# Kernel tuning notes

Hardware: AMD Instinct MI355X
Metric: run time of the kernel (lower is better)

The kernel has to match this reference:

```python
import jax, jax.numpy as jnp
import numpy as np

B = 64        # number of graph segments
BASE = 384    # mean verts per segment
LMAX = 512    # pad length (counts in [256, 512])
H_DIM = 256
H_DIV = 128   # h_dim // h_dim_div
HEADS = 4
DH = H_DIV // HEADS  # 32


def _counts(seed):
    rng = np.random.default_rng(seed)
    d = rng.integers(-128, 129, B)
    d[1::2] = -d[::2]            # paired so the total is exactly B*BASE
    return (BASE + d).astype(np.int64)


def _pad_indices(counts, L):
    # Gather indices/mask mapping packed ragged tokens -> padded [B, L].
    counts = np.asarray(counts)
    off = np.concatenate([[0], np.cumsum(counts)[:-1]])
    ar = np.arange(L)[None, :]
    mask = ar < counts[:, None]
    idx = np.where(mask, off[:, None] + ar, 0)
    return idx, mask


def setup_inputs() -> dict:
    key = jax.random.key(0)
    ks = jax.random.split(key, 16)
    src_num_verts = _counts(0)
    dst_num_verts = _counts(1)
    total = B * BASE  # 24576 for both src and dst

    def w(k, shape):
        return 0.02 * jax.random.normal(k, shape, jnp.float32)

    return {
        'src_h': jax.random.normal(ks[0], (total, H_DIM), jnp.float32),
        'dst_h': jax.random.normal(ks[1], (total, H_DIM), jnp.float32),
        'src_num_verts': src_num_verts,
        'dst_num_verts': dst_num_verts,
        # 1x1 Conv1d == linear over channels
        'Wq': w(ks[2], (H_DIV, H_DIM)), 'bq': w(ks[3], (H_DIV,)),
        'Wk': w(ks[4], (H_DIV, H_DIM)), 'bk': w(ks[5], (H_DIV,)),
        'Wv': w(ks[6], (H_DIV, H_DIM)), 'bv': w(ks[7], (H_DIV,)),
        'Wm': w(ks[8], (H_DIV, H_DIV)), 'bm': w(ks[9], (H_DIV,)),
        'W1': w(ks[10], (H_DIM, H_DIM + H_DIV)), 'b1': w(ks[11], (H_DIM,)),
        'g1': 1.0 + 0.1 * jax.random.normal(ks[12], (H_DIM,), jnp.float32),
        'be1': w(ks[13], (H_DIM,)),
        'rm1': w(ks[14], (H_DIM,)),
        'rv1': jax.random.uniform(ks[15], (H_DIM,), jnp.float32, 0.5, 1.5),
        'W2': w(jax.random.fold_in(key, 100), (H_DIM, H_DIM)),
        'b2': w(jax.random.fold_in(key, 101), (H_DIM,)),
        'g2': 1.0 + 0.1 * jax.random.normal(jax.random.fold_in(key, 102), (H_DIM,), jnp.float32),
        'be2': w(jax.random.fold_in(key, 103), (H_DIM,)),
        'rm2': w(jax.random.fold_in(key, 104), (H_DIM,)),
        'rv2': jax.random.uniform(jax.random.fold_in(key, 105), (H_DIM,), jnp.float32, 0.5, 1.5),
    }


def _bn(x, g, b, rm, rv):
    # BatchNorm1d in eval mode (running stats)
    return (x - rm) / jnp.sqrt(rv + 1e-5) * g + b


def reference(src_h, dst_h, src_num_verts, dst_num_verts,
              Wq, bq, Wk, bk, Wv, bv, Wm, bm,
              W1, b1, g1, be1, rm1, rv1,
              W2, b2, g2, be2, rm2, rv2):
    didx, dmask = _pad_indices(dst_num_verts, LMAX)
    sidx, smask = _pad_indices(src_num_verts, LMAX)

    # fused projections over all packed tokens (1x1 conv == matmul)
    q = src_h_proj = dst_h @ Wq.T + bq        # [Nd, H_DIV]
    k = src_h @ Wk.T + bk                     # [Ns, H_DIV]
    v = src_h @ Wv.T + bv

    # pad to block-diagonal batched form; channel c = d*HEADS + h per torch view
    qp = q[didx].reshape(B, LMAX, DH, HEADS)
    kp = k[sidx].reshape(B, LMAX, DH, HEADS)
    vp = v[sidx].reshape(B, LMAX, DH, HEADS)

    scores = jnp.einsum('bndh,bmdh->bhnm', qp, kp) / (DH ** 0.5)
    scores = jnp.where(jnp.asarray(smask)[:, None, None, :], scores, -1e9)
    attn = jax.nn.softmax(scores, axis=-1)
    msg = jnp.einsum('bhnm,bmdh->bndh', attn, vp).reshape(B, LMAX, H_DIV)
    msg = msg @ Wm.T + bm                     # merge conv

    bb, ii = np.nonzero(dmask)                # unpad back to packed layout
    h_msg = msg[bb, ii]                       # [Nd, H_DIV]

    x = jnp.concatenate([dst_h, h_msg], axis=-1)
    x = _bn(x @ W1.T + b1, g1, be1, rm1, rv1)
    x = jax.nn.relu(x)
    x = _bn(x @ W2.T + b2, g2, be2, rm2, rv2)
    return dst_h + x
```

## Files before the change

kernel.cpp:

```cpp
#include <hip/hip_runtime.h>
#include <hip/hip_bf16.h>
#include <math.h>

#define B_SEG 64
#define HDIM 256
#define HDIV 128
#define NHEADS 4
#define DH 32
#define KSTR 40
#define VSTR 520
#define PSTR 136
#define QSC 0.17677669529663687f

typedef unsigned short u16;
typedef unsigned int u32;

typedef __attribute__((ext_vector_type(8))) short s8v;
typedef __attribute__((ext_vector_type(4))) float f4v;

__device__ __forceinline__ u16 f2bf(float f) {
    u32 v;
    __builtin_memcpy(&v, &f, 4);
    u32 r = v + 0x7fffu + ((v >> 16) & 1u);
    return (u16)(r >> 16);
}

__device__ __forceinline__ void async_cp16(const u16* g, u16* l) {
    __builtin_amdgcn_global_load_lds(
        (const __attribute__((address_space(1))) u32*)g,
        (__attribute__((address_space(3))) u32*)l, 16, 0, 0);
}

__global__ __launch_bounds__(256) void k_prep(
    const float* __restrict__ Wq, const float* __restrict__ bq,
    const float* __restrict__ Wk, const float* __restrict__ bk,
    const float* __restrict__ Wv, const float* __restrict__ bv,
    const float* __restrict__ Wm, const float* __restrict__ bm,
    const float* __restrict__ W1, const float* __restrict__ b1,
    const float* __restrict__ g1, const float* __restrict__ be1,
    const float* __restrict__ rm1, const float* __restrict__ rv1,
    const float* __restrict__ W2, const float* __restrict__ b2,
    const float* __restrict__ g2, const float* __restrict__ be2,
    const float* __restrict__ rm2, const float* __restrict__ rv2,
    const int* __restrict__ sc_raw, const int* __restrict__ dc_raw,
    const float* __restrict__ src_h, const float* __restrict__ dst_h,
    int* __restrict__ meta,
    u16* __restrict__ pWq, u16* __restrict__ pWkv,
    u16* __restrict__ pW1f, u16* __restrict__ pW2,
    float* __restrict__ bqp, float* __restrict__ bkvp,
    float* __restrict__ sc1, float* __restrict__ sh1,
    float* __restrict__ sc2, float* __restrict__ sh2,
    u16* __restrict__ srcb, u16* __restrict__ dstb, int ntot) {
    if (blockIdx.x < 1028) {
        int idx = blockIdx.x * 256 + threadIdx.x;
        if (idx < 32768) {
            int cp = idx >> 8, k = idx & 255;
            int c = ((cp & 31) << 2) | (cp >> 5);
            pWq[idx] = f2bf(Wq[c * 256 + k]);
        } else if (idx < 98304) {
            int i = idx - 32768;
            int rp = i >> 8, k = i & 255;
            int r = rp & 127;
            int c = ((r & 31) << 2) | (r >> 5);
            float v = (rp < 128) ? Wk[c * 256 + k] : Wv[c * 256 + k];
            pWkv[i] = f2bf(v);
        } else if (idx < 163840) {
            int i = idx - 98304;
            int o = i >> 8, k = i & 255;
            pW1f[o * 384 + k] = f2bf(W1[o * 384 + k]);
        } else if (idx < 196608) {
            int i = idx - 163840;
            int o = i >> 7, cp = i & 127;
            int c = ((cp & 31) << 2) | (cp >> 5);
            float acc = 0.f;
            for (int j = 0; j < 128; j++)
                acc += W1[o * 384 + 256 + j] * Wm[j * 128 + c];
            pW1f[o * 384 + 256 + cp] = f2bf(acc);
        } else if (idx < 262144) {
            int i = idx - 196608;
            pW2[i] = f2bf(W2[i]);
        } else if (idx < 263168) {
            int p = idx - 262144;
            if (p < 128) {
                int c = ((p & 31) << 2) | (p >> 5);
                bqp[p] = bq[c] * QSC;
            } else if (p < 384) {
                int r = p - 128; int rr = r & 127;
                int c = ((rr & 31) << 2) | (rr >> 5);
                bkvp[r] = (r < 128) ? bk[c] : bv[c];
            } else if (p < 640) {
                int o = p - 384;
                float bsum = 0.f;
                for (int j = 0; j < 128; j++)
                    bsum += W1[o * 384 + 256 + j] * bm[j];
                float s = g1[o] * rsqrtf(rv1[o] + 1e-5f);
                sc1[o] = s;
                sh1[o] = (b1[o] + bsum - rm1[o]) * s + be1[o];
            } else if (p < 896) {
                int o = p - 640;
                float s = g2[o] * rsqrtf(rv2[o] + 1e-5f);
                sc2[o] = s;
                sh2[o] = (b2[o] - rm2[o]) * s + be2[o];
            }
        }
    } else if (blockIdx.x == 1028) {
        if (threadIdx.x == 0) {
            bool is64 = (sc_raw[1] == 0);
            int so = 0, dofs = 0;
            for (int i = 0; i < B_SEG; i++) {
                int s = is64 ? sc_raw[2 * i] : sc_raw[i];
                int d = is64 ? dc_raw[2 * i] : dc_raw[i];
                meta[i] = s; meta[64 + i] = d;
                meta[128 + i] = so; meta[192 + i] = dofs;
                so += s; dofs += d;
            }
        }
    } else {
        int i = (blockIdx.x - 1029) * 256 + threadIdx.x;
        int half = ntot * 64;
        const float4* s;
        u16* o;
        int j = i;
        if (i < half) { s = (const float4*)src_h; o = srcb; }
        else { s = (const float4*)dst_h; o = dstb; j = i - half; }
        float4 v = s[j];
        ushort4 u = {f2bf(v.x), f2bf(v.y), f2bf(v.z), f2bf(v.w)};
        ((ushort4*)o)[j] = u;
    }
}

__device__ __forceinline__ void gemm_body(
    const u16* __restrict__ A, int lda,
    const u16* __restrict__ A2, int lda2, int K1,
    const u16* __restrict__ Bw, int K, int m0, int n0,
    const float* __restrict__ scale, const float* __restrict__ shift,
    const float* __restrict__ resid,
    void* __restrict__ Cout, int ldc, int flags,
    u16* Al, u16* Bl) {
    int tid = threadIdx.x;
    int w = tid >> 6, lane = tid & 63;
    int wm = w & 1, wn = w >> 1;
    int l15 = lane & 15, quad = lane >> 4;
    int srow = w * 32 + (lane >> 2);
    int scol = (lane & 3) << 3;
    u16* al0 = Al + w * 1024;
    u16* bl0 = Bl + w * 1024;
    f4v acc[4][4] = {};

    for (int k0 = 0; k0 < K; k0 += 32) {
        const u16* Ag; int aL, acol;
        if (k0 < K1) { Ag = A; aL = lda; acol = k0; }
        else { Ag = A2; aL = lda2; acol = k0 - K1; }
        async_cp16(&Ag[(size_t)(m0 + srow) * aL + acol + scol], al0);
        async_cp16(&Ag[(size_t)(m0 + srow + 16) * aL + acol + scol], al0 + 512);
        async_cp16(&Bw[(size_t)(n0 + srow) * K + k0 + scol], bl0);
        async_cp16(&Bw[(size_t)(n0 + srow + 16) * K + k0 + scol], bl0 + 512);
        __syncthreads();
        s8v af[4], bf[4];
#pragma unroll
        for (int i = 0; i < 4; i++)
            af[i] = *(const s8v*)(&Al[(wm * 64 + i * 16 + l15) * 32 + quad * 8]);
#pragma unroll
        for (int j = 0; j < 4; j++)
            bf[j] = *(const s8v*)(&Bl[(wn * 64 + j * 16 + l15) * 32 + quad * 8]);
#pragma unroll
        for (int i = 0; i < 4; i++)
#pragma unroll
            for (int j = 0; j < 4; j++)
                acc[i][j] = __builtin_amdgcn_mfma_f32_16x16x32_bf16(
                    af[i], bf[j], acc[i][j], 0, 0, 0);
        __syncthreads();
    }
#pragma unroll
    for (int i = 0; i < 4; i++) {
#pragma unroll
        for (int j = 0; j < 4; j++) {
            int n = n0 + wn * 64 + j * 16 + l15;
            float sc = scale ? scale[n] : 1.f;
            float sh = shift ? shift[n] : 0.f;
#pragma unroll
            for (int r = 0; r < 4; r++) {
                int m = m0 + wm * 64 + i * 16 + quad * 4 + r;
                float v = acc[i][j][r];
                if (flags & 4) v *= QSC;
                v = v * sc + sh;
                if (flags & 1) v = fmaxf(v, 0.f);
                if (resid) v += resid[(size_t)m * 256 + n];
                if (flags & 2) ((float*)Cout)[(size_t)m * ldc + n] = v;
                else ((u16*)Cout)[(size_t)m * ldc + n] = f2bf(v);
            }
        }
    }
}

__global__ __launch_bounds__(256) void k_qkv(
    const u16* __restrict__ dstb, const u16* __restrict__ srcb,
    const u16* __restrict__ pWq, const u16* __restrict__ pWkv,
    const float* __restrict__ bqp, const float* __restrict__ bkvp,
    u16* __restrict__ qb, u16* __restrict__ kvb) {
    __shared__ u16 Al[4096];
    __shared__ u16 Bl[4096];
    int m0 = blockIdx.x * 128;
    if (blockIdx.y == 0)
        gemm_body(dstb, 256, dstb, 256, 256, pWq, 256, m0, 0,
                  nullptr, bqp, nullptr, qb, 128, 4, Al, Bl);
    else
        gemm_body(srcb, 256, srcb, 256, 256, pWkv, 256, m0, (blockIdx.y - 1) * 128,
                  nullptr, bkvp, nullptr, kvb, 256, 0, Al, Bl);
}

__global__ __launch_bounds__(256) void k_gemm(
    const u16* __restrict__ A, int lda,
    const u16* __restrict__ A2, int lda2, int K1,
    const u16* __restrict__ Bw, int K,
    const float* __restrict__ scale, const float* __restrict__ shift,
    const float* __restrict__ resid,
    void* __restrict__ Cout, int ldc, int flags) {
    __shared__ u16 Al[4096];
    __shared__ u16 Bl[4096];
    gemm_body(A, lda, A2, lda2, K1, Bw, K, blockIdx.x * 128, blockIdx.y * 128,
              scale, shift, resid, Cout, ldc, flags, Al, Bl);
}

__global__ __launch_bounds__(512, 2) void k_attn(
    const u16* __restrict__ qb, const u16* __restrict__ kvb,
    const int* __restrict__ meta, u16* __restrict__ msgb) {
    extern __shared__ u16 sm[];
    u16* Kl = sm;
    u16* Vl = sm + 512 * KSTR;
    u16* Pl = Vl + 32 * VSTR;
    int b = blockIdx.x, h = blockIdx.y;
    int ns = meta[b], nd = meta[64 + b];
    int soff = meta[128 + b], doff = meta[192 + b];
    int tid = threadIdx.x, w = tid >> 6, lane = tid & 63;
    int l15 = lane & 15, quad = lane >> 4;

    {
        int m = tid;
        if (m < ns) {
            const uint4* ks = (const uint4*)&kvb[(size_t)(soff + m) * 256 + h * 32];
#pragma unroll
            for (int q4 = 0; q4 < 4; q4++)
                *(uint4*)&Kl[m * KSTR + q4 * 8] = ks[q4];
            uint4 vv[4];
            const uint4* vs = (const uint4*)&kvb[(size_t)(soff + m) * 256 + 128 + h * 32];
#pragma unroll
            for (int q4 = 0; q4 < 4; q4++) vv[q4] = vs[q4];
            const u16* pv = (const u16*)vv;
#pragma unroll
            for (int d = 0; d < 32; d++) Vl[d * VSTR + m] = pv[d];
        } else {
#pragma unroll
            for (int d = 0; d < 32; d++) Vl[d * VSTR + m] = 0;
        }
    }
    __syncthreads();

    int nt = (ns + 15) >> 4;
    int nc = (ns + 127) >> 7;
    u16* Pw = Pl + w * 16 * PSTR;

    for (int s0 = w * 16; s0 < nd; s0 += 128) {
        int qr = min(s0 + l15, nd - 1);
        s8v aq = *(const s8v*)&qb[(size_t)(doff + qr) * 128 + h * 32 + quad * 8];

        f4v e[32];
        float lsum[4] = {0.f, 0.f, 0.f, 0.f};
#pragma unroll
        for (int t = 0; t < 32; t++) {
            if (t < nt) {
                int kr = t * 16 + l15;
                s8v bk = *(const s8v*)&Kl[kr * KSTR + quad * 8];
                f4v s_ = __builtin_amdgcn_mfma_f32_16x16x32_bf16(
                    aq, bk, (f4v){0.f, 0.f, 0.f, 0.f}, 0, 0, 0);
                bool ok = kr < ns;
#pragma unroll
                for (int r = 0; r < 4; r++) {
                    float ev = ok ? __expf(s_[r]) : 0.f;
                    e[t][r] = ev;
                    lsum[r] += ev;
                }
            } else {
#pragma unroll
                for (int r = 0; r < 4; r++) e[t][r] = 0.f;
            }
        }
        float inv[4];
#pragma unroll
        for (int r = 0; r < 4; r++) {
            float s_ = lsum[r];
#pragma unroll
            for (int x = 1; x < 16; x <<= 1) s_ += __shfl_xor(s_, x, 16);
            inv[r] = 1.f / s_;
        }

        f4v oa0 = {0.f, 0.f, 0.f, 0.f}, oa1 = {0.f, 0.f, 0.f, 0.f};
#pragma unroll
        for (int c = 0; c < 4; c++) {
            if (c < nc) {
#pragma unroll
                for (int tt = 0; tt < 8; tt++)
#pragma unroll
                    for (int r = 0; r < 4; r++)
                        Pw[(quad * 4 + r) * PSTR + tt * 16 + l15] =
                            f2bf(e[c * 8 + tt][r]);
#pragma unroll
                for (int kc = 0; kc < 4; kc++) {
                    s8v ap = *(const s8v*)&Pw[l15 * PSTR + kc * 32 + quad * 8];
                    s8v bv0 = *(const s8v*)&Vl[l15 * VSTR + c * 128 + kc * 32 + quad * 8];
                    s8v bv1 = *(const s8v*)&Vl[(16 + l15) * VSTR + c * 128 + kc * 32 + quad * 8];
                    oa0 = __builtin_amdgcn_mfma_f32_16x16x32_bf16(ap, bv0, oa0, 0, 0, 0);
                    oa1 = __builtin_amdgcn_mfma_f32_16x16x32_bf16(ap, bv1, oa1, 0, 0, 0);
                }
            }
        }
#pragma unroll
        for (int r = 0; r < 4; r++) {
            int row = s0 + quad * 4 + r;
            if (row < nd) {
                size_t base = (size_t)(doff + row) * 128 + h * 32;
                msgb[base + l15] = f2bf(oa0[r] * inv[r]);
                msgb[base + 16 + l15] = f2bf(oa1[r] * inv[r]);
            }
        }
    }
}

extern "C" void kernel_launch(void* const* d_in, const int* in_sizes, int n_in,
                              void* d_out, int out_size, void* d_ws, size_t ws_size,
                              hipStream_t stream) {
    const float* src_h = (const float*)d_in[0];
    const float* dst_h = (const float*)d_in[1];
    const int* snv = (const int*)d_in[2];
    const int* dnv = (const int*)d_in[3];
    const float* Wq = (const float*)d_in[4];  const float* bq = (const float*)d_in[5];
    const float* Wk = (const float*)d_in[6];  const float* bk = (const float*)d_in[7];
    const float* Wv = (const float*)d_in[8];  const float* bv = (const float*)d_in[9];
    const float* Wm = (const float*)d_in[10]; const float* bm = (const float*)d_in[11];
    const float* W1 = (const float*)d_in[12]; const float* b1 = (const float*)d_in[13];
    const float* g1 = (const float*)d_in[14]; const float* be1 = (const float*)d_in[15];
    const float* rm1 = (const float*)d_in[16]; const float* rv1 = (const float*)d_in[17];
    const float* W2 = (const float*)d_in[18]; const float* b2 = (const float*)d_in[19];
    const float* g2 = (const float*)d_in[20]; const float* be2 = (const float*)d_in[21];
    const float* rm2 = (const float*)d_in[22]; const float* rv2 = (const float*)d_in[23];

    int ntot = out_size / HDIM;
    int mt = ntot / 128;

    char* ws = (char*)d_ws;
    int* meta = (int*)ws;
    float* bqp = (float*)(ws + 4096);
    float* bkvp = (float*)(ws + 4608);
    float* sc1 = (float*)(ws + 6144);
    float* sh1 = (float*)(ws + 7168);
    float* sc2 = (float*)(ws + 8192);
    float* sh2 = (float*)(ws + 9216);
    u16* pWq = (u16*)(ws + 16384);
    u16* pWkv = (u16*)(ws + 81920);
    u16* pW1f = (u16*)(ws + 212992);
    u16* pW2 = (u16*)(ws + 409600);
    u16* srcb = (u16*)(ws + 1048576);
    u16* x1b = srcb;
    u16* dstb = (u16*)(ws + 13631488);

    u16* qb = (u16*)d_out;
    u16* kvb = qb + (size_t)ntot * 128;
    u16* msgb = kvb + (size_t)ntot * 256;

    hipFuncSetAttribute((const void*)k_attn,
                        hipFuncAttributeMaxDynamicSharedMemorySize, 131072);

    k_prep<<<dim3(1029 + ntot / 2), dim3(256), 0, stream>>>(
        Wq, bq, Wk, bk, Wv, bv, Wm, bm, W1, b1, g1, be1, rm1, rv1,
        W2, b2, g2, be2, rm2, rv2, snv, dnv, src_h, dst_h, meta,
        pWq, pWkv, pW1f, pW2, bqp, bkvp, sc1, sh1, sc2, sh2,
        srcb, dstb, ntot);
    k_qkv<<<dim3(mt, 3), dim3(256), 0, stream>>>(
        dstb, srcb, pWq, pWkv, bqp, bkvp, qb, kvb);
    k_attn<<<dim3(B_SEG, NHEADS), dim3(512), 109056, stream>>>(qb, kvb, meta, msgb);
    k_gemm<<<dim3(mt, 2), dim3(256), 0, stream>>>(
        dstb, 256, msgb, 128, 256, pW1f, 384, sc1, sh1, nullptr, x1b, 256, 1);
    k_gemm<<<dim3(mt, 2), dim3(256), 0, stream>>>(
        x1b, 256, x1b, 256, 256, pW2, 256, sc2, sh2, dst_h, d_out, 256, 2);
}
```

Before: 232.6 us.

## Fuse the two MLP GEMMs into one kernel, keeping the hidden tile in LDS

The two k_gemm launches (W1 with BN and ReLU, then W2 with BN and the residual add) are replaced by a single k_mlp kernel. Each block computes a 64-row tile across all 256 output columns and stores the bf16 hidden activations in a swizzled LDS buffer, then runs the second GEMM straight from LDS. This removes the global write and re-read of the intermediate x1 tensor and one kernel launch. msgb moves into the workspace because the output buffer is now written while msgb is still being read. The cost is more LDS per block (about 52 KB) and a k-loop that loads and computes in sequence rather than overlapping, which may limit occupancy and latency hiding.

```diff
diff --git a/kernel.cpp b/kernel.cpp
--- a/kernel.cpp
+++ b/kernel.cpp
@@ -209,17 +209,115 @@
                   nullptr, bkvp, nullptr, kvb, 256, 0, Al, Bl);
 }
 
-__global__ __launch_bounds__(256) void k_gemm(
-    const u16* __restrict__ A, int lda,
-    const u16* __restrict__ A2, int lda2, int K1,
-    const u16* __restrict__ Bw, int K,
-    const float* __restrict__ scale, const float* __restrict__ shift,
-    const float* __restrict__ resid,
-    void* __restrict__ Cout, int ldc, int flags) {
-    __shared__ u16 Al[4096];
-    __shared__ u16 Bl[4096];
-    gemm_body(A, lda, A2, lda2, K1, Bw, K, blockIdx.x * 128, blockIdx.y * 128,
-              scale, shift, resid, Cout, ldc, flags, Al, Bl);
+__global__ __launch_bounds__(256) void k_mlp(
+    const u16* __restrict__ dstb, const u16* __restrict__ msgb,
+    const u16* __restrict__ pW1f, const u16* __restrict__ pW2,
+    const float* __restrict__ sc1, const float* __restrict__ sh1,
+    const float* __restrict__ sc2, const float* __restrict__ sh2,
+    const float* __restrict__ dst_h, float* __restrict__ out) {
+    __shared__ u16 Al[64 * 32];
+    __shared__ u16 Bl[256 * 32];
+    __shared__ u16 X1[64 * 256];
+    int m0 = blockIdx.x * 64;
+    int tid = threadIdx.x;
+    int w = tid >> 6, lane = tid & 63;
+    int wm = w & 1, wn = w >> 1;
+    int l15 = lane & 15, quad = lane >> 4;
+    int srow = w * 16 + (lane >> 2);
+    int scol = (lane & 3) << 3;
+    u16* al0 = Al + w * 512;
+    f4v acc[2][8];
+
+#pragma unroll
+    for (int i = 0; i < 2; i++)
+#pragma unroll
+        for (int j = 0; j < 8; j++) acc[i][j] = (f4v){0.f, 0.f, 0.f, 0.f};
+
+    for (int k0 = 0; k0 < 384; k0 += 32) {
+        const u16* Ag; int aL, acol;
+        if (k0 < 256) { Ag = dstb; aL = 256; acol = k0; }
+        else { Ag = msgb; aL = 128; acol = k0 - 256; }
+        async_cp16(&Ag[(size_t)(m0 + srow) * aL + acol + scol], al0);
+#pragma unroll
+        for (int c = 0; c < 4; c++)
+            async_cp16(&pW1f[(size_t)(c * 64 + srow) * 384 + k0 + scol],
+                       Bl + c * 2048 + w * 512);
+        __syncthreads();
+        s8v af[2], bf[8];
+#pragma unroll
+        for (int i = 0; i < 2; i++)
+            af[i] = *(const s8v*)(&Al[(wm * 32 + i * 16 + l15) * 32 + quad * 8]);
+#pragma unroll
+        for (int j = 0; j < 8; j++)
+            bf[j] = *(const s8v*)(&Bl[(wn * 128 + j * 16 + l15) * 32 + quad * 8]);
+#pragma unroll
+        for (int i = 0; i < 2; i++)
+#pragma unroll
+            for (int j = 0; j < 8; j++)
+                acc[i][j] = __builtin_amdgcn_mfma_f32_16x16x32_bf16(
+                    af[i], bf[j], acc[i][j], 0, 0, 0);
+        __syncthreads();
+    }
+#pragma unroll
+    for (int i = 0; i < 2; i++) {
+#pragma unroll
+        for (int j = 0; j < 8; j++) {
+            int n = wn * 128 + j * 16 + l15;
+            float sc = sc1[n], sh = sh1[n];
+#pragma unroll
+            for (int r = 0; r < 4; r++) {
+                int row = wm * 32 + i * 16 + quad * 4 + r;
+                float v = fmaxf(acc[i][j][r] * sc + sh, 0.f);
+                int sl = (n >> 3) ^ (row & 7);
+                X1[row * 256 + sl * 8 + (n & 7)] = f2bf(v);
+            }
+        }
+    }
+    __syncthreads();
+
+#pragma unroll
+    for (int i = 0; i < 2; i++)
+#pragma unroll
+        for (int j = 0; j < 8; j++) acc[i][j] = (f4v){0.f, 0.f, 0.f, 0.f};
+
+    for (int k0 = 0; k0 < 256; k0 += 32) {
+#pragma unroll
+        for (int c = 0; c < 4; c++)
+            async_cp16(&pW2[(size_t)(c * 64 + srow) * 256 + k0 + scol],
+                       Bl + c * 2048 + w * 512);
+        __syncthreads();
+        s8v af[2], bf[8];
+#pragma unroll
+        for (int i = 0; i < 2; i++) {
+            int row = wm * 32 + i * 16 + l15;
+            int sl = ((k0 >> 3) + quad) ^ (row & 7);
+            af[i] = *(const s8v*)(&X1[row * 256 + sl * 8]);
+        }
+#pragma unroll
+        for (int j = 0; j < 8; j++)
+            bf[j] = *(const s8v*)(&Bl[(wn * 128 + j * 16 + l15) * 32 + quad * 8]);
+#pragma unroll
+        for (int i = 0; i < 2; i++)
+#pragma unroll
+            for (int j = 0; j < 8; j++)
+                acc[i][j] = __builtin_amdgcn_mfma_f32_16x16x32_bf16(
+                    af[i], bf[j], acc[i][j], 0, 0, 0);
+        __syncthreads();
+    }
+#pragma unroll
+    for (int i = 0; i < 2; i++) {
+#pragma unroll
+        for (int j = 0; j < 8; j++) {
+            int n = wn * 128 + j * 16 + l15;
+            float sc = sc2[n], sh = sh2[n];
+#pragma unroll
+            for (int r = 0; r < 4; r++) {
+                int m = m0 + wm * 32 + i * 16 + quad * 4 + r;
+                float v = acc[i][j][r] * sc + sh + dst_h[(size_t)m * 256 + n];
+                out[(size_t)m * 256 + n] = v;
+            }
+        }
+    }
 }
 
 __global__ __launch_bounds__(512, 2) void k_attn(
@@ -360,12 +458,11 @@
     u16* pW1f = (u16*)(ws + 212992);
     u16* pW2 = (u16*)(ws + 409600);
     u16* srcb = (u16*)(ws + 1048576);
-    u16* x1b = srcb;
     u16* dstb = (u16*)(ws + 13631488);
+    u16* msgb = (u16*)(ws + 26214400);
 
     u16* qb = (u16*)d_out;
     u16* kvb = qb + (size_t)ntot * 128;
-    u16* msgb = kvb + (size_t)ntot * 256;
 
     hipFuncSetAttribute((const void*)k_attn,
                         hipFuncAttributeMaxDynamicSharedMemorySize, 131072);
@@ -378,8 +475,6 @@
     k_qkv<<<dim3(mt, 3), dim3(256), 0, stream>>>(
         dstb, srcb, pWq, pWkv, bqp, bkvp, qb, kvb);
     k_attn<<<dim3(B_SEG, NHEADS), dim3(512), 109056, stream>>>(qb, kvb, meta, msgb);
-    k_gemm<<<dim3(mt, 2), dim3(256), 0, stream>>>(
-        dstb, 256, msgb, 128, 256, pW1f, 384, sc1, sh1, nullptr, x1b, 256, 1);
-    k_gemm<<<dim3(mt, 2), dim3(256), 0, stream>>>(
-        x1b, 256, x1b, 256, 256, pW2, 256, sc2, sh2, dst_h, d_out, 256, 2);
-}
+    k_mlp<<<dim3(ntot / 64), dim3(256), 0, stream>>>(
+        dstb, msgb, pW1f, pW2, sc1, sh1, sc2, sh2, dst_h, (float*)d_out);
+}
```

New measurement: 220.5 us. 5.2% less time.
